# Kernel optimization log

Hardware: AMD Instinct MI355X
Metric: run time of the kernel (lower is better)

Reference implementation:

```python
import jax, jax.numpy as jnp
import numpy as np

N_NODES = 20000
N_EDGES = 640000
IN_NODE = 128
IN_EDGE = 16
HIDDEN = 64
OUT = 128
HEADS = 4
N_GRAPHS = 64
NEG_SLOPE = 0.2


def _glorot(key, shape):
    fan_in, fan_out = shape[0], shape[-1]
    s = jnp.sqrt(6.0 / (fan_in + fan_out)).astype(jnp.float32)
    return jax.random.uniform(key, shape, jnp.float32, -s, s)


def setup_inputs() -> dict:
    key = jax.random.key(0)
    ks = jax.random.split(key, 32)
    inp = {
        "x": jax.random.normal(ks[0], (N_NODES, IN_NODE), jnp.float32),
        "edge_attr": jax.random.normal(ks[1], (N_EDGES, IN_EDGE), jnp.float32),
        "edge_index": jax.random.randint(ks[2], (2, N_EDGES), 0, N_NODES),
        "batch": jnp.sort(jax.random.randint(ks[3], (N_NODES,), 0, N_GRAPHS)),
    }
    # layer dims: (in, out_per_head, concat)
    dims = [(IN_NODE, HIDDEN, True), (HIDDEN * HEADS, HIDDEN, True), (HIDDEN * HEADS, OUT, False)]
    k = 4
    for i, (cin, cout, concat) in enumerate(dims):
        hc = HEADS * cout
        inp[f"Wl{i}"] = _glorot(ks[k], (cin, hc)); k += 1
        inp[f"bl{i}"] = jnp.zeros((hc,), jnp.float32)
        inp[f"Wr{i}"] = _glorot(ks[k], (cin, hc)); k += 1
        inp[f"br{i}"] = jnp.zeros((hc,), jnp.float32)
        inp[f"We{i}"] = _glorot(ks[k], (IN_EDGE, hc)); k += 1
        inp[f"att{i}"] = _glorot(ks[k], (HEADS, cout)); k += 1
        inp[f"bias{i}"] = jnp.zeros((hc if concat else cout,), jnp.float32)
    return inp


def _gatv2_layer(x, edge_index, edge_attr, Wl, bl, Wr, br, We, att, bias, concat):
    """One PyG-style GATv2Conv layer with edge features."""
    H, C = att.shape
    N = x.shape[0]
    src, dst = edge_index[0], edge_index[1]
    xl = (x @ Wl + bl).reshape(N, H, C)  # messages from source
    xr = (x @ Wr + br).reshape(N, H, C)  # target query
    e = (edge_attr @ We).reshape(-1, H, C)
    m = jax.nn.leaky_relu(xl[src] + xr[dst] + e, NEG_SLOPE)  # [E,H,C]
    logits = jnp.einsum("ehc,hc->eh", m, att)  # [E,H]
    # scatter-softmax over edges grouped by destination node
    lmax = jax.ops.segment_max(logits, dst, num_segments=N)
    p = jnp.exp(logits - lmax[dst])
    denom = jax.ops.segment_sum(p, dst, num_segments=N)
    alpha = p / (denom[dst] + 1e-16)  # [E,H]
    out = jax.ops.segment_sum(alpha[:, :, None] * xl[src], dst, num_segments=N)  # [N,H,C]
    if concat:
        return out.reshape(N, H * C) + bias
    return out.mean(axis=1) + bias


def reference(x, edge_attr, edge_index, batch,
              Wl0, bl0, Wr0, br0, We0, att0, bias0,
              Wl1, bl1, Wr1, br1, We1, att1, bias1,
              Wl2, bl2, Wr2, br2, We2, att2, bias2):
    layers = [
        (Wl0, bl0, Wr0, br0, We0, att0, bias0, True),
        (Wl1, bl1, Wr1, br1, We1, att1, bias1, True),
        (Wl2, bl2, Wr2, br2, We2, att2, bias2, False),
    ]
    h = x
    for (Wl, bl, Wr, br, We, att, b, concat) in layers:
        h = _gatv2_layer(h, edge_index, edge_attr, Wl, bl, Wr, br, We, att, b, concat)
    # global max + mean pooling per graph
    x_max = jax.ops.segment_max(h, batch, num_segments=N_GRAPHS)
    s = jax.ops.segment_sum(h, batch, num_segments=N_GRAPHS)
    cnt = jax.ops.segment_sum(jnp.ones((h.shape[0], 1), h.dtype), batch, num_segments=N_GRAPHS)
    x_mean = s / jnp.maximum(cnt, 1.0)
    return jnp.concatenate([x_max, x_mean], axis=1)  # [G, 2*OUT]
```

## Files before the change

kernel.cpp:

```cpp
#include <hip/hip_runtime.h>

#define NB 8

typedef float f32x2 __attribute__((ext_vector_type(2)));

template <int HI>
__device__ __forceinline__ void pkfma_b(f32x2& d, const f32x2 x, const f32x2 w) {
  if constexpr (HI == 0)
    asm("v_pk_fma_f32 %0, %1, %2, %0 op_sel:[0,0,0] op_sel_hi:[0,1,1]"
        : "+v"(d) : "v"(x), "v"(w));
  else
    asm("v_pk_fma_f32 %0, %1, %2, %0 op_sel:[1,0,0] op_sel_hi:[1,1,1]"
        : "+v"(d) : "v"(x), "v"(w));
}

template <int K, int M, int NPB>
__global__ __launch_bounds__(256) void node_gemm2(
    const float* __restrict__ X, const float* __restrict__ W1,
    const float* __restrict__ b1, float* __restrict__ Y1,
    const float* __restrict__ W2, const float* __restrict__ b2,
    float* __restrict__ Y2, int nodeBlocks) {
  constexpr int COLS4 = M / 4;
  constexpr int NG = 256 / COLS4;
  constexpr int RPN = NPB / NG;
  __shared__ float xs[NPB * K];
  const int tid = threadIdx.x;
  const int hi = blockIdx.x >= nodeBlocks;
  const float* W = hi ? W2 : W1;
  const float* bias = hi ? b2 : b1;
  float* Y = hi ? Y2 : Y1;
  const int n0 = (hi ? blockIdx.x - nodeBlocks : blockIdx.x) * NPB;
  {
    const float4* X4 = reinterpret_cast<const float4*>(X + (size_t)n0 * K);
    float4* xs4 = reinterpret_cast<float4*>(xs);
    for (int i = tid; i < NPB * K / 4; i += 256) xs4[i] = X4[i];
  }
  __syncthreads();
  const int c4 = (tid % COLS4) * 4;
  const int r0 = (tid / COLS4) * RPN;
  f32x2 acc[RPN][2];
#pragma unroll
  for (int r = 0; r < RPN; ++r)
#pragma unroll
    for (int q = 0; q < 2; ++q) acc[r][q] = (f32x2)(0.f);

  for (int k = 0; k < K; k += 4) {
    f32x2 xp[RPN][2];
#pragma unroll
    for (int r = 0; r < RPN; ++r) {
      const float4 t = *reinterpret_cast<const float4*>(&xs[(r0 + r) * K + k]);
      xp[r][0].x = t.x; xp[r][0].y = t.y;
      xp[r][1].x = t.z; xp[r][1].y = t.w;
    }
#pragma unroll
    for (int j2 = 0; j2 < 2; ++j2) {
      const float4 t0 =
          *reinterpret_cast<const float4*>(&W[(size_t)(k + 2 * j2) * M + c4]);
      const float4 t1 =
          *reinterpret_cast<const float4*>(&W[(size_t)(k + 2 * j2 + 1) * M + c4]);
      f32x2 w0a, w0b, w1a, w1b;
      w0a.x = t0.x; w0a.y = t0.y; w0b.x = t0.z; w0b.y = t0.w;
      w1a.x = t1.x; w1a.y = t1.y; w1b.x = t1.z; w1b.y = t1.w;
#pragma unroll
      for (int r = 0; r < RPN; ++r) {
        pkfma_b<0>(acc[r][0], xp[r][j2], w0a);
        pkfma_b<0>(acc[r][1], xp[r][j2], w0b);
        pkfma_b<1>(acc[r][0], xp[r][j2], w1a);
        pkfma_b<1>(acc[r][1], xp[r][j2], w1b);
      }
    }
  }
  float bv[4];
  *reinterpret_cast<float4*>(bv) = *reinterpret_cast<const float4*>(&bias[c4]);
#pragma unroll
  for (int r = 0; r < RPN; ++r) {
    float o[4];
    o[0] = acc[r][0].x + bv[0];
    o[1] = acc[r][0].y + bv[1];
    o[2] = acc[r][1].x + bv[2];
    o[3] = acc[r][1].y + bv[3];
    *reinterpret_cast<float4*>(&Y[(size_t)(n0 + r0 + r) * M + c4]) =
        *reinterpret_cast<float4*>(o);
  }
}

__global__ void hist_b(const int* __restrict__ ei, int* __restrict__ kcnt,
                       const int* __restrict__ batch, int* __restrict__ gstart,
                       int* __restrict__ gend, int E, int N, int bdiv) {
  int i = blockIdx.x * blockDim.x + threadIdx.x;
  if (i < E) atomicAdd(&kcnt[ei[E + i] * NB + ei[i] / bdiv], 1);
  if (i < N) {
    int g = batch[i];
    atomicMin(&gstart[g], i);
    atomicMax(&gend[g], i + 1);
  }
}

__global__ __launch_bounds__(1024) void blk_scan(
    const int* __restrict__ in, int* __restrict__ out1, int* __restrict__ bsum, int n) {
  __shared__ int buf[1024];
  const int tid = threadIdx.x;
  const int gid = blockIdx.x * 1024 + tid;
  int v = (gid < n) ? in[gid] : 0;
  buf[tid] = v;
  __syncthreads();
  for (int off = 1; off < 1024; off <<= 1) {
    int t = (tid >= off) ? buf[tid - off] : 0;
    __syncthreads();
    buf[tid] += t;
    __syncthreads();
  }
  if (gid < n) out1[gid] = buf[tid];
  if (tid == 1023) bsum[blockIdx.x] = buf[1023];
}

__global__ __launch_bounds__(256) void scan_bsum(int* __restrict__ bsum, int nb) {
  __shared__ int buf[256];
  const int tid = threadIdx.x;
  int v = (tid < nb) ? bsum[tid] : 0;
  buf[tid] = v;
  __syncthreads();
  for (int off = 1; off < 256; off <<= 1) {
    int t = (tid >= off) ? buf[tid - off] : 0;
    __syncthreads();
    buf[tid] += t;
    __syncthreads();
  }
  if (tid < nb) bsum[tid] = buf[tid];
}

__global__ void add_off(int* __restrict__ kptr, const int* __restrict__ bsum, int n) {
  int gid = blockIdx.x * blockDim.x + threadIdx.x;
  if (gid == 0) kptr[0] = 0;
  if (gid < n) {
    int blk = gid >> 10;
    if (blk > 0) kptr[1 + gid] += bsum[blk - 1];
  }
}

__global__ void csr_fill_b(const int* __restrict__ ei, const int* __restrict__ kptr,
                           int* __restrict__ kfill, int* __restrict__ csr_src,
                           const float* __restrict__ ea, float* __restrict__ ea_csr,
                           int E, int bdiv) {
  int i = blockIdx.x * blockDim.x + threadIdx.x;
  if (i < E) {
    int src = ei[i], dst = ei[E + i];
    int key = dst * NB + src / bdiv;
    int slot = kptr[key] + atomicAdd(&kfill[key], 1);
    csr_src[slot] = src;
    const float4* es = reinterpret_cast<const float4*>(ea) + (size_t)i * 4;
    float4* ed = reinterpret_cast<float4*>(ea_csr) + (size_t)slot * 4;
    float4 v0 = es[0], v1 = es[1], v2 = es[2], v3 = es[3];
    ed[0] = v0; ed[1] = v1; ed[2] = v2; ed[3] = v3;
  }
}

template <int GS>
__device__ __forceinline__ void gat_edge_s(
    const float4 a, const float (&c)[16], const float4 xv,
    const float (&wef)[16][4], const float (&attv)[4],
    float& m, float& s, float (&acc)[4]) {
  float mv[4] = {a.x + xv.x, a.y + xv.y, a.z + xv.z, a.w + xv.w};
#pragma unroll
  for (int k = 0; k < 16; ++k) {
#pragma unroll
    for (int q = 0; q < 4; ++q) mv[q] = fmaf(c[k], wef[k][q], mv[q]);
  }
  float l = 0.f;
#pragma unroll
  for (int q = 0; q < 4; ++q) {
    const float v = fmaxf(mv[q], 0.2f * mv[q]);
    l = fmaf(v, attv[q], l);
  }
#pragma unroll
  for (int off = 1; off < GS; off <<= 1) l += __shfl_xor(l, off);
  const float nm = fmaxf(m, l);
  const float sc = __expf(m - nm);
  const float pe = __expf(l - nm);
  m = nm;
  s = fmaf(s, sc, pe);
  acc[0] = fmaf(pe, a.x, acc[0] * sc);
  acc[1] = fmaf(pe, a.y, acc[1] * sc);
  acc[2] = fmaf(pe, a.z, acc[2] * sc);
  acc[3] = fmaf(pe, a.w, acc[3] * sc);
}

template <int HCROW, int MODE>
__global__ __launch_bounds__(256) void fused_gat(
    const float* __restrict__ xl, const float* __restrict__ xr,
    const float* __restrict__ ea_csr, const float* __restrict__ We,
    const float* __restrict__ att, const float* __restrict__ bias,
    const int* __restrict__ kptr, const int* __restrict__ csr_src,
    float* __restrict__ out, float* __restrict__ outB, int N) {
  constexpr int C = HCROW / 4;
  constexpr int GS = C / 4;
  const int lane = threadIdx.x & 63;
  const int wslot = threadIdx.x >> 6;
  int bx = blockIdx.x;
  int colbase = 0;
  float* o_ptr = out;
  if (MODE == 1) {
    const int gb = gridDim.x >> 1;
    if (bx >= gb) { bx -= gb; colbase = 256; o_ptr = outB; }
  }
  const int dst = bx * 4 + wslot;
  if (dst >= N) return;

  float wef[16][4];
#pragma unroll
  for (int k = 0; k < 16; ++k)
    *reinterpret_cast<float4*>(wef[k]) =
        *reinterpret_cast<const float4*>(&We[k * HCROW + colbase + lane * 4]);
  const int col0 = colbase + lane * 4;
  const int head = col0 / C;
  float attv[4];
  *reinterpret_cast<float4*>(attv) =
      *reinterpret_cast<const float4*>(&att[head * C + (col0 % C)]);
  const float4* xl4 = reinterpret_cast<const float4*>(xl);
  const int rs4 = HCROW / 4;
  const int coff = col0 >> 2;
  const float4 xrv =
      reinterpret_cast<const float4*>(xr)[(size_t)dst * rs4 + coff];

  const int row0 = __builtin_amdgcn_readfirstlane(kptr[dst * NB]);
  const int rend = __builtin_amdgcn_readfirstlane(kptr[dst * NB + NB]);

  float m = -__builtin_inff(), s = 0.f;
  float acc[4] = {0.f, 0.f, 0.f, 0.f};

  if (row0 < rend) {
    const int last = rend - 1;
    const int s0 = csr_src[row0];
    const int s1 = csr_src[min(row0 + 1, last)];
    const int s2 = csr_src[min(row0 + 2, last)];
    const int s3 = csr_src[min(row0 + 3, last)];
    float4 a0 = xl4[(size_t)s0 * rs4 + coff];
    float4 a1 = xl4[(size_t)s1 * rs4 + coff];
    float4 a2 = xl4[(size_t)s2 * rs4 + coff];
    float4 a3 = xl4[(size_t)s3 * rs4 + coff];
    int sr0 = csr_src[min(row0 + 4, last)];
    int sr1 = csr_src[min(row0 + 5, last)];
    float c0[16], c1[16];
    {
      const float* e0 = ea_csr + (size_t)row0 * 16;
      const float* e1 = ea_csr + (size_t)min(row0 + 1, last) * 16;
#pragma unroll
      for (int k = 0; k < 16; ++k) { c0[k] = e0[k]; c1[k] = e1[k]; }
    }

    for (int p = row0; p < rend; p += 2) {
      const float4 na0 = xl4[(size_t)sr0 * rs4 + coff];
      const float4 na1 = xl4[(size_t)sr1 * rs4 + coff];
      const int nsr0 = csr_src[min(p + 6, last)];
      const int nsr1 = csr_src[min(p + 7, last)];
      float cn0[16], cn1[16];
      {
        const float* e0 = ea_csr + (size_t)min(p + 2, last) * 16;
        const float* e1 = ea_csr + (size_t)min(p + 3, last) * 16;
#pragma unroll
        for (int k = 0; k < 16; ++k) { cn0[k] = e0[k]; cn1[k] = e1[k]; }
      }
      gat_edge_s<GS>(a0, c0, xrv, wef, attv, m, s, acc);
      if (p + 1 < rend) gat_edge_s<GS>(a1, c1, xrv, wef, attv, m, s, acc);
      a0 = a2; a1 = a3; a2 = na0; a3 = na1;
      sr0 = nsr0; sr1 = nsr1;
#pragma unroll
      for (int k = 0; k < 16; ++k) { c0[k] = cn0[k]; c1[k] = cn1[k]; }
    }
  }

  const float inv = 1.f / (s + 1e-16f);
  float o[4];
  if (MODE == 0) {
    float bv[4];
    *reinterpret_cast<float4*>(bv) = *reinterpret_cast<const float4*>(&bias[col0]);
#pragma unroll
    for (int q = 0; q < 4; ++q) o[q] = fmaf(acc[q], inv, bv[q]);
    *reinterpret_cast<float4*>(&o_ptr[(size_t)dst * HCROW + col0]) =
        *reinterpret_cast<float4*>(o);
  } else {
#pragma unroll
    for (int q = 0; q < 4; ++q) {
      o[q] = acc[q] * inv;
      o[q] += __shfl_xor(o[q], 32);
    }
    if (lane < 32)
      *reinterpret_cast<float4*>(&o_ptr[(size_t)dst * 128 + lane * 4]) =
          *reinterpret_cast<float4*>(o);
  }
}

__global__ __launch_bounds__(256) void pool_graph(
    const float* __restrict__ hA, const float* __restrict__ hB,
    const float* __restrict__ bias2, const int* __restrict__ gstart,
    const int* __restrict__ gend, float* __restrict__ out) {
  const int g = blockIdx.x;
  const int c = threadIdx.x & 127;
  const int sub = threadIdx.x >> 7;
  const int s0 = gstart[g], e0 = gend[g];
  const float b = bias2[c];
  float mx = -__builtin_inff(), sm = 0.f;
  for (int n = s0 + sub; n < e0; n += 2) {
    const float v = fmaf(0.25f, hA[(size_t)n * 128 + c] + hB[(size_t)n * 128 + c], b);
    mx = fmaxf(mx, v);
    sm += v;
  }
  __shared__ float smx[128], ssm[128];
  if (sub) { smx[c] = mx; ssm[c] = sm; }
  __syncthreads();
  if (!sub) {
    mx = fmaxf(mx, smx[c]);
    sm += ssm[c];
    const int cnt = e0 - s0;
    out[g * 256 + c] = (cnt > 0) ? mx : 0.f;
    out[g * 256 + 128 + c] = sm / fmaxf((float)cnt, 1.f);
  }
}

extern "C" void kernel_launch(void* const* d_in, const int* in_sizes, int n_in,
                              void* d_out, int out_size, void* d_ws, size_t ws_size,
                              hipStream_t stream) {
  const float* x     = (const float*)d_in[0];
  const float* ea    = (const float*)d_in[1];
  const int*   ei    = (const int*)d_in[2];
  const int*   batch = (const int*)d_in[3];
  const int N = in_sizes[0] / 128;
  const int E = in_sizes[2] / 2;
  const int NBINS = N * NB;
  const int bdiv = (N + NB - 1) / NB;

  const float* Wl[3]   = {(const float*)d_in[4],  (const float*)d_in[11], (const float*)d_in[18]};
  const float* blv[3]  = {(const float*)d_in[5],  (const float*)d_in[12], (const float*)d_in[19]};
  const float* Wr[3]   = {(const float*)d_in[6],  (const float*)d_in[13], (const float*)d_in[20]};
  const float* brv[3]  = {(const float*)d_in[7],  (const float*)d_in[14], (const float*)d_in[21]};
  const float* Wev[3]  = {(const float*)d_in[8],  (const float*)d_in[15], (const float*)d_in[22]};
  const float* attv[3] = {(const float*)d_in[9],  (const float*)d_in[16], (const float*)d_in[23]};
  const float* bias[3] = {(const float*)d_in[10], (const float*)d_in[17], (const float*)d_in[24]};

  float* ws = (float*)d_ws;
  float* xl     = ws;
  float* xr     = xl + (size_t)N * 512;
  float* ea_csr = xr + (size_t)N * 512;
  float* h      = ea_csr + (size_t)E * 16;
  int* kptr     = (int*)(h + (size_t)N * 256);
  int* csr_src  = kptr + (NBINS + 1);
  int* bsum     = csr_src + E;
  int* gstart   = bsum + 257;
  int* gend     = gstart + 64;
  int* kcnt    = (int*)h;
  int* kfill   = kcnt + NBINS;
  float* hsumA = h;
  float* hsumB = h + (size_t)N * 128;
  (void)n_in; (void)out_size; (void)ws_size;

  const int edgeBlocks = (E + 255) / 256;
  const int scanBlocks = (NBINS + 1023) / 1024;
  const int gatBlocks = (N + 3) / 4;
  const int nb32 = N / 32;
  const int nb16 = N / 16;

  hipMemsetAsync(kcnt, 0, (size_t)2 * NBINS * sizeof(int), stream);
  hipMemsetAsync(gstart, 0x7f, 64 * sizeof(int), stream);
  hipMemsetAsync(gend, 0, 64 * sizeof(int), stream);
  hist_b<<<edgeBlocks, 256, 0, stream>>>(ei, kcnt, batch, gstart, gend, E, N, bdiv);
  blk_scan<<<scanBlocks, 1024, 0, stream>>>(kcnt, kptr + 1, bsum, NBINS);
  scan_bsum<<<1, 256, 0, stream>>>(bsum, scanBlocks);
  add_off<<<(NBINS + 255) / 256, 256, 0, stream>>>(kptr, bsum, NBINS);
  csr_fill_b<<<edgeBlocks, 256, 0, stream>>>(ei, kptr, kfill, csr_src, ea, ea_csr, E, bdiv);

  node_gemm2<128, 256, 32><<<2 * nb32, 256, 0, stream>>>(
      x, Wl[0], blv[0], xl, Wr[0], brv[0], xr, nb32);
  fused_gat<256, 0><<<gatBlocks, 256, 0, stream>>>(
      xl, xr, ea_csr, Wev[0], attv[0], bias[0], kptr, csr_src, h, nullptr, N);

  node_gemm2<256, 256, 32><<<2 * nb32, 256, 0, stream>>>(
      h, Wl[1], blv[1], xl, Wr[1], brv[1], xr, nb32);
  fused_gat<256, 0><<<gatBlocks, 256, 0, stream>>>(
      xl, xr, ea_csr, Wev[1], attv[1], bias[1], kptr, csr_src, h, nullptr, N);

  node_gemm2<256, 512, 16><<<2 * nb16, 256, 0, stream>>>(
      h, Wl[2], blv[2], xl, Wr[2], brv[2], xr, nb16);
  fused_gat<512, 1><<<2 * gatBlocks, 256, 0, stream>>>(
      xl, xr, ea_csr, Wev[2], attv[2], bias[2], kptr, csr_src, hsumA, hsumB, N);

  pool_graph<<<64, 256, 0, stream>>>(hsumA, hsumB, bias[2], gstart, gend, (float*)d_out);
}
```

Baseline: 1.008 ms.

## Stage weight chunks in shared memory and enlarge node tiles in node GEMM

The node GEMM now copies K-chunks of the weight matrix into LDS cooperatively and reads weights from there instead of from global memory in every thread. Node tile sizes are increased (40 nodes per block for the first two layers, 32 for the last) so each staged weight chunk is reused across more rows. This trades extra LDS usage and per-chunk barriers, and higher register pressure from more rows per thread, for less global/L2 weight traffic.

After: 1.038 ms. +3.0%, slower.

```diff
diff --git a/kernel.cpp b/kernel.cpp
--- a/kernel.cpp
+++ b/kernel.cpp
@@ -14,7 +14,7 @@
         : "+v"(d) : "v"(x), "v"(w));
 }
 
-template <int K, int M, int NPB>
+template <int K, int M, int NPB, int KC>
 __global__ __launch_bounds__(256) void node_gemm2(
     const float* __restrict__ X, const float* __restrict__ W1,
     const float* __restrict__ b1, float* __restrict__ Y1,
@@ -24,6 +24,7 @@
   constexpr int NG = 256 / COLS4;
   constexpr int RPN = NPB / NG;
   __shared__ float xs[NPB * K];
+  __shared__ float wsh[KC * M];
   const int tid = threadIdx.x;
   const int hi = blockIdx.x >= nodeBlocks;
   const float* W = hi ? W2 : W1;
@@ -35,7 +36,6 @@
     float4* xs4 = reinterpret_cast<float4*>(xs);
     for (int i = tid; i < NPB * K / 4; i += 256) xs4[i] = X4[i];
   }
-  __syncthreads();
   const int c4 = (tid % COLS4) * 4;
   const int r0 = (tid / COLS4) * RPN;
   f32x2 acc[RPN][2];
@@ -44,29 +44,38 @@
 #pragma unroll
     for (int q = 0; q < 2; ++q) acc[r][q] = (f32x2)(0.f);
 
-  for (int k = 0; k < K; k += 4) {
-    f32x2 xp[RPN][2];
-#pragma unroll
-    for (int r = 0; r < RPN; ++r) {
-      const float4 t = *reinterpret_cast<const float4*>(&xs[(r0 + r) * K + k]);
-      xp[r][0].x = t.x; xp[r][0].y = t.y;
-      xp[r][1].x = t.z; xp[r][1].y = t.w;
-    }
-#pragma unroll
-    for (int j2 = 0; j2 < 2; ++j2) {
-      const float4 t0 =
-          *reinterpret_cast<const float4*>(&W[(size_t)(k + 2 * j2) * M + c4]);
-      const float4 t1 =
-          *reinterpret_cast<const float4*>(&W[(size_t)(k + 2 * j2 + 1) * M + c4]);
-      f32x2 w0a, w0b, w1a, w1b;
-      w0a.x = t0.x; w0a.y = t0.y; w0b.x = t0.z; w0b.y = t0.w;
-      w1a.x = t1.x; w1a.y = t1.y; w1b.x = t1.z; w1b.y = t1.w;
+  for (int kc = 0; kc < K; kc += KC) {
+    __syncthreads();
+    {
+      const float4* Wg = reinterpret_cast<const float4*>(W + (size_t)kc * M);
+      float4* ws4 = reinterpret_cast<float4*>(wsh);
+#pragma unroll
+      for (int i = tid; i < KC * M / 4; i += 256) ws4[i] = Wg[i];
+    }
+    __syncthreads();
+#pragma unroll
+    for (int k = 0; k < KC; k += 4) {
+      f32x2 w[4][2];
+#pragma unroll
+      for (int j = 0; j < 4; ++j) {
+        const float4 t = *reinterpret_cast<const float4*>(&wsh[(k + j) * M + c4]);
+        w[j][0].x = t.x; w[j][0].y = t.y;
+        w[j][1].x = t.z; w[j][1].y = t.w;
+      }
 #pragma unroll
       for (int r = 0; r < RPN; ++r) {
-        pkfma_b<0>(acc[r][0], xp[r][j2], w0a);
-        pkfma_b<0>(acc[r][1], xp[r][j2], w0b);
-        pkfma_b<1>(acc[r][0], xp[r][j2], w1a);
-        pkfma_b<1>(acc[r][1], xp[r][j2], w1b);
+        const float4 t =
+            *reinterpret_cast<const float4*>(&xs[(r0 + r) * K + kc + k]);
+        f32x2 x01, x23;
+        x01.x = t.x; x01.y = t.y; x23.x = t.z; x23.y = t.w;
+        pkfma_b<0>(acc[r][0], x01, w[0][0]);
+        pkfma_b<0>(acc[r][1], x01, w[0][1]);
+        pkfma_b<1>(acc[r][0], x01, w[1][0]);
+        pkfma_b<1>(acc[r][1], x01, w[1][1]);
+        pkfma_b<0>(acc[r][0], x23, w[2][0]);
+        pkfma_b<0>(acc[r][1], x23, w[2][1]);
+        pkfma_b<1>(acc[r][0], x23, w[3][0]);
+        pkfma_b<1>(acc[r][1], x23, w[3][1]);
       }
     }
   }
@@ -356,8 +365,8 @@
   const int edgeBlocks = (E + 255) / 256;
   const int scanBlocks = (NBINS + 1023) / 1024;
   const int gatBlocks = (N + 3) / 4;
+  const int nb40 = N / 40;
   const int nb32 = N / 32;
-  const int nb16 = N / 16;
 
   hipMemsetAsync(kcnt, 0, (size_t)2 * NBINS * sizeof(int), stream);
   hipMemsetAsync(gstart, 0x7f, 64 * sizeof(int), stream);
@@ -368,18 +377,18 @@
   add_off<<<(NBINS + 255) / 256, 256, 0, stream>>>(kptr, bsum, NBINS);
   csr_fill_b<<<edgeBlocks, 256, 0, stream>>>(ei, kptr, kfill, csr_src, ea, ea_csr, E, bdiv);
 
-  node_gemm2<128, 256, 32><<<2 * nb32, 256, 0, stream>>>(
-      x, Wl[0], blv[0], xl, Wr[0], brv[0], xr, nb32);
+  node_gemm2<128, 256, 40, 32><<<2 * nb40, 256, 0, stream>>>(
+      x, Wl[0], blv[0], xl, Wr[0], brv[0], xr, nb40);
   fused_gat<256, 0><<<gatBlocks, 256, 0, stream>>>(
       xl, xr, ea_csr, Wev[0], attv[0], bias[0], kptr, csr_src, h, nullptr, N);
 
-  node_gemm2<256, 256, 32><<<2 * nb32, 256, 0, stream>>>(
-      h, Wl[1], blv[1], xl, Wr[1], brv[1], xr, nb32);
+  node_gemm2<256, 256, 40, 32><<<2 * nb40, 256, 0, stream>>>(
+      h, Wl[1], blv[1], xl, Wr[1], brv[1], xr, nb40);
   fused_gat<256, 0><<<gatBlocks, 256, 0, stream>>>(
       xl, xr, ea_csr, Wev[1], attv[1], bias[1], kptr, csr_src, h, nullptr, N);
 
-  node_gemm2<256, 512, 16><<<2 * nb16, 256, 0, stream>>>(
-      h, Wl[2], blv[2], xl, Wr[2], brv[2], xr, nb16);
+  node_gemm2<256, 512, 32, 16><<<2 * nb32, 256, 0, stream>>>(
+      h, Wl[2], blv[2], xl, Wr[2], brv[2], xr, nb32);
   fused_gat<512, 1><<<2 * gatBlocks, 256, 0, stream>>>(
       xl, xr, ea_csr, Wev[2], attv[2], bias[2], kptr, csr_src, hsumA, hsumB, N);
 
```
